# Kernel tuning notes

Hardware: AMD Instinct MI355X
Metric: run time of the kernel (lower is better)

The kernel has to match this reference:

```python
import jax, jax.numpy as jnp
import numpy as np

POOLING_COUNTS = [15, 8, 8]
N = 64


def _build_specs():
    # Reproduces SparseMaxPool.__init__: mask2d and per-pooler (kernel, stride, i, j).
    mask = np.zeros((N, N), dtype=bool)
    mask[np.arange(N), np.arange(N)] = True
    stride, offset = 1, 0
    specs = []
    for idx, c in enumerate(POOLING_COUNTS):
        for t in range(c):
            offset += stride
            i = np.arange(0, N - offset, stride)
            j = np.arange(offset, N, stride)
            mask[i, j] = True
            # first pooler of each later scale group is MaxPool1d(3,2), rest are (2,1)
            k, s = (3, 2) if (idx > 0 and t == 0) else (2, 1)
            specs.append((k, s, i, j))
        stride *= 2
    return mask, specs


def _maxpool1d(x, k, s):
    # x: [B, D, L] -> [B, D, (L-k)//s + 1], max over sliding window via strided slices
    L = x.shape[-1]
    out = (L - k) // s + 1
    y = x[..., 0:s * (out - 1) + 1:s]
    for d in range(1, k):
        y = jnp.maximum(y, x[..., d:d + s * (out - 1) + 1:s])
    return y


def setup_inputs() -> dict:
    key = jax.random.key(0)
    return {"x": jax.random.normal(key, (32, 512, N), dtype=jnp.float32)}


def reference(x):
    mask_np, specs = _build_specs()
    B, D, n = x.shape
    diag = jnp.arange(n)
    map2d = jnp.zeros((B, D, n, n), dtype=x.dtype).at[:, :, diag, diag].set(x)
    for k, s, i, j in specs:
        x = _maxpool1d(x, k, s)
        map2d = map2d.at[:, :, jnp.asarray(i), jnp.asarray(j)].set(x)
    mask2d = jnp.broadcast_to(jnp.asarray(mask_np)[None, None], (B, 1, n, n))
    return map2d, mask2d
```

## Files before the change

kernel.cpp:

```cpp
#include <hip/hip_runtime.h>


typedef unsigned int u32;

__device__ __constant__ int SPEC_LEN[31] = {
  63,62,61,60,59,58,57,56,55,54,53,52,51,50,49,
  24,23,22,21,20,19,18,17,
  8,7,6,5,4,3,2,1};
__device__ __constant__ int SPEC_BASE[31] = {
  64,127,189,250,310,369,427,484,540,595,649,702,754,805,855,
  904,928,951,973,994,1014,1033,1051,
  1068,1076,1083,1089,1094,1098,1101,1103};

#define E(base, sh) ((base) | ((sh) << 16) | (1 << 24))
__device__ __constant__ int DTAB[64] = {
  E(0,0),   E(64,0),  E(127,0), E(189,0), E(250,0), E(310,0), E(369,0), E(427,0),
  E(484,0), E(540,0), E(595,0), E(649,0), E(702,0), E(754,0), E(805,0), E(855,0),
  0,        E(904,1), 0,        E(928,1), 0,        E(951,1), 0,        E(973,1),
  0,        E(994,1), 0,        E(1014,1),0,        E(1033,1),0,        E(1051,1),
  0, 0, 0,  E(1068,2),0, 0, 0,  E(1076,2),0, 0, 0,  E(1083,2),0, 0, 0,  E(1089,2),
  0, 0, 0,  E(1094,2),0, 0, 0,  E(1098,2),0, 0, 0,  E(1101,2),0, 0, 0,  E(1103,2)
};
#undef E

__device__ __forceinline__ float tile_elem(const float* v, const int* dt, int r, int c) {
  const int d = c - r;
  if (d < 0) return 0.f;
  const int e  = dt[d];
  const int sh = (e >> 16) & 0xFF;
  if (e != 0 && ((r & ((1 << sh) - 1)) == 0)) return v[(e & 0xFFFF) + (r >> sh)];
  return 0.f;
}

__global__ void __launch_bounds__(256)
pool_map_kernel(const float* __restrict__ x, float* __restrict__ out) {
  __shared__ float vals[4][1104];
  __shared__ int dtab[64];

  const int tid  = threadIdx.x;
  const int w    = tid >> 6;
  const int lane = tid & 63;
  if (tid < 64) dtab[tid] = DTAB[tid];

  const int row = blockIdx.x * 4 + w;
  float cur = x[(size_t)row * 64 + lane];
  vals[w][lane] = cur;

#pragma unroll
  for (int m = 0; m < 31; ++m) {
    if (m == 15 || m == 23) {
      float a = __shfl(cur, 2 * lane);
      float b = __shfl(cur, 2 * lane + 1);
      float c = __shfl(cur, 2 * lane + 2);
      cur = fmaxf(fmaxf(a, b), c);
    } else {
      cur = fmaxf(cur, __shfl_down(cur, 1));
    }
    if (lane < SPEC_LEN[m]) vals[w][SPEC_BASE[m] + lane] = cur;
  }
  __syncthreads();

  const float* v = vals[w];
  float* orow = out + (size_t)row * 4096;
#pragma unroll
  for (int it = 0; it < 16; ++it) {
    const int f  = it * 256 + lane * 4;
    const int r  = f >> 6;
    const int c0 = f & 63;
    float4 o;
    o.x = tile_elem(v, dtab, r, c0);
    o.y = tile_elem(v, dtab, r, c0 + 1);
    o.z = tile_elem(v, dtab, r, c0 + 2);
    o.w = tile_elem(v, dtab, r, c0 + 3);
    *(float4*)(orow + f) = o;
  }
}

__device__ __forceinline__ float mask_val(int r, int c) {
  const int d = c - r;
  if (d < 0) return 0.f;
  const int e  = DTAB[d];
  const int sh = (e >> 16) & 0xFF;
  return (e != 0 && ((r & ((1 << sh) - 1)) == 0)) ? 1.f : 0.f;
}

__global__ void __launch_bounds__(256)
mask_kernel(float* __restrict__ out, int nvec) {
  const int i = blockIdx.x * 256 + threadIdx.x;
  if (i >= nvec) return;
  const int f  = (i * 4) & 4095;
  const int r  = f >> 6;
  const int c0 = f & 63;
  float4 o;
  o.x = mask_val(r, c0);
  o.y = mask_val(r, c0 + 1);
  o.z = mask_val(r, c0 + 2);
  o.w = mask_val(r, c0 + 3);
  *(float4*)(out + (size_t)i * 4) = o;
}

extern "C" void kernel_launch(void* const* d_in, const int* in_sizes, int n_in,
                              void* d_out, int out_size, void* d_ws, size_t ws_size,
                              hipStream_t stream) {
  const float* x = (const float*)d_in[0];
  float* out = (float*)d_out;

  const int nx    = in_sizes[0];
  const int nrows = nx / 64;
  const int B     = out_size / 4096 - nrows;

  pool_map_kernel<<<dim3(nrows / 4), 256, 0, stream>>>(x, out);

  float* omask = out + (size_t)nrows * 4096;
  const int nvec = (B * 4096) / 4;
  mask_kernel<<<dim3((nvec + 255) / 256), 256, 0, stream>>>(omask, nvec);
}
```

Measured before the change: 266.2 us.

## Precompute per-block LDS gather index table and use persistent grid loop

```diff
diff --git a/kernel.cpp b/kernel.cpp
--- a/kernel.cpp
+++ b/kernel.cpp
@@ -1,7 +1,8 @@
 #include <hip/hip_runtime.h>
 
 
-typedef unsigned int u32;
+typedef unsigned short u16;
+typedef unsigned int   u32;
 
 __device__ __constant__ int SPEC_LEN[31] = {
   63,62,61,60,59,58,57,56,55,54,53,52,51,50,49,
@@ -23,56 +24,63 @@
 };
 #undef E
 
-__device__ __forceinline__ float tile_elem(const float* v, const int* dt, int r, int c) {
-  const int d = c - r;
-  if (d < 0) return 0.f;
-  const int e  = dt[d];
-  const int sh = (e >> 16) & 0xFF;
-  if (e != 0 && ((r & ((1 << sh) - 1)) == 0)) return v[(e & 0xFFFF) + (r >> sh)];
-  return 0.f;
-}
-
-__global__ void __launch_bounds__(256)
-pool_map_kernel(const float* __restrict__ x, float* __restrict__ out) {
-  __shared__ float vals[4][1104];
-  __shared__ int dtab[64];
+__global__ void __launch_bounds__(256, 6)
+pool_map_kernel(const float* __restrict__ x, float* __restrict__ out, int ngroups) {
+  __shared__ float vals[4][1112];
+  __shared__ u16 idx[4096];
 
   const int tid  = threadIdx.x;
   const int w    = tid >> 6;
   const int lane = tid & 63;
-  if (tid < 64) dtab[tid] = DTAB[tid];
-
-  const int row = blockIdx.x * 4 + w;
-  float cur = x[(size_t)row * 64 + lane];
-  vals[w][lane] = cur;
 
 #pragma unroll
-  for (int m = 0; m < 31; ++m) {
-    if (m == 15 || m == 23) {
-      float a = __shfl(cur, 2 * lane);
-      float b = __shfl(cur, 2 * lane + 1);
-      float c = __shfl(cur, 2 * lane + 2);
-      cur = fmaxf(fmaxf(a, b), c);
-    } else {
-      cur = fmaxf(cur, __shfl_down(cur, 1));
+  for (int k = 0; k < 16; ++k) {
+    const int f = tid + k * 256;
+    const int r = f >> 6, c = f & 63, d = c - r;
+    u16 off = 4416;
+    if (d >= 0) {
+      const int e  = DTAB[d];
+      const int sh = (e >> 16) & 0xFF;
+      if (e != 0 && ((r & ((1 << sh) - 1)) == 0))
+        off = (u16)(((e & 0xFFFF) + (r >> sh)) * 4);
     }
-    if (lane < SPEC_LEN[m]) vals[w][SPEC_BASE[m] + lane] = cur;
+    idx[f] = off;
   }
+  if (lane < 8) vals[w][1104 + lane] = 0.f;
   __syncthreads();
 
-  const float* v = vals[w];
-  float* orow = out + (size_t)row * 4096;
+  const char* valsw = (const char*)&vals[w][0];
+
+  for (int grp = blockIdx.x; grp < ngroups; grp += gridDim.x) {
+    const int row = grp * 4 + w;
+    float cur = x[(size_t)row * 64 + lane];
+    vals[w][lane] = cur;
+
 #pragma unroll
-  for (int it = 0; it < 16; ++it) {
-    const int f  = it * 256 + lane * 4;
-    const int r  = f >> 6;
-    const int c0 = f & 63;
-    float4 o;
-    o.x = tile_elem(v, dtab, r, c0);
-    o.y = tile_elem(v, dtab, r, c0 + 1);
-    o.z = tile_elem(v, dtab, r, c0 + 2);
-    o.w = tile_elem(v, dtab, r, c0 + 3);
-    *(float4*)(orow + f) = o;
+    for (int m = 0; m < 31; ++m) {
+      if (m == 15 || m == 23) {
+        float a = __shfl(cur, 2 * lane);
+        float b = __shfl(cur, 2 * lane + 1);
+        float c = __shfl(cur, 2 * lane + 2);
+        cur = fmaxf(fmaxf(a, b), c);
+      } else {
+        cur = fmaxf(cur, __shfl_down(cur, 1));
+      }
+      if (lane < SPEC_LEN[m]) vals[w][SPEC_BASE[m] + lane] = cur;
+    }
+
+    float* orow = out + (size_t)row * 4096;
+#pragma unroll 4
+    for (int it = 0; it < 16; ++it) {
+      const int f = it * 256 + lane * 4;
+      const uint2 p = *(const uint2*)&idx[f];
+      float4 o;
+      o.x = *(const float*)(valsw + (p.x & 0xFFFFu));
+      o.y = *(const float*)(valsw + (p.x >> 16));
+      o.z = *(const float*)(valsw + (p.y & 0xFFFFu));
+      o.w = *(const float*)(valsw + (p.y >> 16));
+      *(float4*)(orow + f) = o;
+    }
   }
 }
 
@@ -105,11 +113,12 @@
   const float* x = (const float*)d_in[0];
   float* out = (float*)d_out;
 
-  const int nx    = in_sizes[0];
-  const int nrows = nx / 64;
-  const int B     = out_size / 4096 - nrows;
+  const int nx      = in_sizes[0];
+  const int nrows   = nx / 64;
+  const int ngroups = nrows / 4;
+  const int B       = out_size / 4096 - nrows;
 
-  pool_map_kernel<<<dim3(nrows / 4), 256, 0, stream>>>(x, out);
+  pool_map_kernel<<<dim3(2048), 256, 0, stream>>>(x, out, ngroups);
 
   float* omask = out + (size_t)nrows * 4096;
   const int nvec = (B * 4096) / 4;
```

After: 304.1 us. +14.3%, slower.

## Fuse map and mask into one wave-per-tile kernel with LDS tile copy

Applied to the files above, without the earlier changes.

```diff
diff --git a/kernel.cpp b/kernel.cpp
--- a/kernel.cpp
+++ b/kernel.cpp
@@ -1,102 +1,63 @@
 #include <hip/hip_runtime.h>
 
 
-typedef unsigned int u32;
-
-__device__ __constant__ int SPEC_LEN[31] = {
+constexpr int S_LEN[31] = {
   63,62,61,60,59,58,57,56,55,54,53,52,51,50,49,
   24,23,22,21,20,19,18,17,
   8,7,6,5,4,3,2,1};
-__device__ __constant__ int SPEC_BASE[31] = {
-  64,127,189,250,310,369,427,484,540,595,649,702,754,805,855,
-  904,928,951,973,994,1014,1033,1051,
-  1068,1076,1083,1089,1094,1098,1101,1103};
+constexpr int S_ST[31] = {
+  1,1,1,1,1,1,1,1,1,1,1,1,1,1,1,
+  2,2,2,2,2,2,2,2,
+  4,4,4,4,4,4,4,4};
+constexpr int S_OFF[31] = {
+  1,2,3,4,5,6,7,8,9,10,11,12,13,14,15,
+  17,19,21,23,25,27,29,31,
+  35,39,43,47,51,55,59,63};
 
-#define E(base, sh) ((base) | ((sh) << 16) | (1 << 24))
-__device__ __constant__ int DTAB[64] = {
-  E(0,0),   E(64,0),  E(127,0), E(189,0), E(250,0), E(310,0), E(369,0), E(427,0),
-  E(484,0), E(540,0), E(595,0), E(649,0), E(702,0), E(754,0), E(805,0), E(855,0),
-  0,        E(904,1), 0,        E(928,1), 0,        E(951,1), 0,        E(973,1),
-  0,        E(994,1), 0,        E(1014,1),0,        E(1033,1),0,        E(1051,1),
-  0, 0, 0,  E(1068,2),0, 0, 0,  E(1076,2),0, 0, 0,  E(1083,2),0, 0, 0,  E(1089,2),
-  0, 0, 0,  E(1094,2),0, 0, 0,  E(1098,2),0, 0, 0,  E(1101,2),0, 0, 0,  E(1103,2)
-};
-#undef E
+__global__ void __launch_bounds__(64)
+sparse_pool_kernel(const float* __restrict__ x, float* __restrict__ out,
+                   int nrows, int ntiles) {
+  __shared__ float tile[4096];
+  const int lane = threadIdx.x;
 
-__device__ __forceinline__ float tile_elem(const float* v, const int* dt, int r, int c) {
-  const int d = c - r;
-  if (d < 0) return 0.f;
-  const int e  = dt[d];
-  const int sh = (e >> 16) & 0xFF;
-  if (e != 0 && ((r & ((1 << sh) - 1)) == 0)) return v[(e & 0xFFFF) + (r >> sh)];
-  return 0.f;
-}
+  const float4 z = make_float4(0.f, 0.f, 0.f, 0.f);
+#pragma unroll
+  for (int i = 0; i < 16; ++i)
+    ((float4*)tile)[i * 64 + lane] = z;
 
-__global__ void __launch_bounds__(256)
-pool_map_kernel(const float* __restrict__ x, float* __restrict__ out) {
-  __shared__ float vals[4][1104];
-  __shared__ int dtab[64];
+  int t = blockIdx.x;
+  float curx = 0.f;
+  if (t < ntiles) curx = (t < nrows) ? x[(size_t)t * 64 + lane] : 1.0f;
 
-  const int tid  = threadIdx.x;
-  const int w    = tid >> 6;
-  const int lane = tid & 63;
-  if (tid < 64) dtab[tid] = DTAB[tid];
+  for (; t < ntiles; t += gridDim.x) {
+    tile[lane * 65] = curx;
 
-  const int row = blockIdx.x * 4 + w;
-  float cur = x[(size_t)row * 64 + lane];
-  vals[w][lane] = cur;
+    float cur = curx;
+#pragma unroll
+    for (int m = 0; m < 31; ++m) {
+      if (m == 15 || m == 23) {
+        float a = __shfl(cur, 2 * lane);
+        float b = __shfl(cur, 2 * lane + 1);
+        float c = __shfl(cur, 2 * lane + 2);
+        cur = fmaxf(fmaxf(a, b), c);
+      } else {
+        cur = fmaxf(cur, __shfl_down(cur, 1));
+      }
+      if (lane < S_LEN[m]) tile[lane * (S_ST[m] * 65) + S_OFF[m]] = cur;
+    }
 
+    const int tn = t + gridDim.x;
+    float nx = 0.f;
+    if (tn < ntiles) nx = (tn < nrows) ? x[(size_t)tn * 64 + lane] : 1.0f;
+
+    float4* o4 = (float4*)(out + (size_t)t * 4096);
+    const float4* t4 = (const float4*)tile;
 #pragma unroll
-  for (int m = 0; m < 31; ++m) {
-    if (m == 15 || m == 23) {
-      float a = __shfl(cur, 2 * lane);
-      float b = __shfl(cur, 2 * lane + 1);
-      float c = __shfl(cur, 2 * lane + 2);
-      cur = fmaxf(fmaxf(a, b), c);
-    } else {
-      cur = fmaxf(cur, __shfl_down(cur, 1));
-    }
-    if (lane < SPEC_LEN[m]) vals[w][SPEC_BASE[m] + lane] = cur;
+    for (int it = 0; it < 16; ++it)
+      o4[it * 64 + lane] = t4[it * 64 + lane];
+
+    curx = nx;
   }
-  __syncthreads();
-
-  const float* v = vals[w];
-  float* orow = out + (size_t)row * 4096;
-#pragma unroll
-  for (int it = 0; it < 16; ++it) {
-    const int f  = it * 256 + lane * 4;
-    const int r  = f >> 6;
-    const int c0 = f & 63;
-    float4 o;
-    o.x = tile_elem(v, dtab, r, c0);
-    o.y = tile_elem(v, dtab, r, c0 + 1);
-    o.z = tile_elem(v, dtab, r, c0 + 2);
-    o.w = tile_elem(v, dtab, r, c0 + 3);
-    *(float4*)(orow + f) = o;
-  }
-}
-
-__device__ __forceinline__ float mask_val(int r, int c) {
-  const int d = c - r;
-  if (d < 0) return 0.f;
-  const int e  = DTAB[d];
-  const int sh = (e >> 16) & 0xFF;
-  return (e != 0 && ((r & ((1 << sh) - 1)) == 0)) ? 1.f : 0.f;
-}
-
-__global__ void __launch_bounds__(256)
-mask_kernel(float* __restrict__ out, int nvec) {
-  const int i = blockIdx.x * 256 + threadIdx.x;
-  if (i >= nvec) return;
-  const int f  = (i * 4) & 4095;
-  const int r  = f >> 6;
-  const int c0 = f & 63;
-  float4 o;
-  o.x = mask_val(r, c0);
-  o.y = mask_val(r, c0 + 1);
-  o.z = mask_val(r, c0 + 2);
-  o.w = mask_val(r, c0 + 3);
-  *(float4*)(out + (size_t)i * 4) = o;
 }
 
 extern "C" void kernel_launch(void* const* d_in, const int* in_sizes, int n_in,
@@ -105,13 +66,10 @@
   const float* x = (const float*)d_in[0];
   float* out = (float*)d_out;
 
-  const int nx    = in_sizes[0];
-  const int nrows = nx / 64;
-  const int B     = out_size / 4096 - nrows;
+  const int nx     = in_sizes[0];
+  const int nrows  = nx / 64;
+  const int ntiles = out_size / 4096;
 
-  pool_map_kernel<<<dim3(nrows / 4), 256, 0, stream>>>(x, out);
-
-  float* omask = out + (size_t)nrows * 4096;
-  const int nvec = (B * 4096) / 4;
-  mask_kernel<<<dim3((nvec + 255) / 256), 256, 0, stream>>>(omask, nvec);
+  const int blocks = (ntiles + 7) / 8;
+  sparse_pool_kernel<<<dim3(blocks), 64, 0, stream>>>(x, out, nrows, ntiles);
 }
```

Measured after the change: 266.7 us, median of 2. Within noise of the previous version (+0.2%).
